# Performance work log

Hardware: AMD Instinct MI355X
Metric: run time of the kernel (lower is better)

Reference implementation:

```python
import jax, jax.numpy as jnp
import numpy as np

EPS = 1e-5  # batch-norm epsilon


def subm_conv(feat, nbrs, W):
    # feat: [N, Cin], nbrs: [N, K] int indices into feat (rulebook), W: [K, Cin, Cout]
    gathered = feat[nbrs]                      # [N, K, Cin]  irregular gather
    return jnp.einsum('nkc,kcd->nd', gathered, W)


def batch_norm(f, gamma, beta):
    # training-mode BN over active sites (scn.BatchNormalization semantics)
    mean = jnp.mean(f, axis=0)
    var = jnp.var(f, axis=0)
    return (f - mean) * jax.lax.rsqrt(var + EPS) * gamma + beta


def setup_inputs() -> dict:
    key = jax.random.key(0)
    k1, k2, k3, k4 = jax.random.split(key, 4)
    N, K, C = 300000, 9, 64
    scale = 1.0 / np.sqrt(K * C)
    return {
        'x': jax.random.normal(k1, (N, C), dtype=jnp.float32),
        'nbrs': jax.random.randint(k2, (N, K), 0, N, dtype=jnp.int32),
        'W1': jax.random.normal(k3, (K, C, C), dtype=jnp.float32) * scale,
        'gamma1': jnp.ones((C,), jnp.float32),
        'beta1': jnp.zeros((C,), jnp.float32),
        'W2': jax.random.normal(k4, (K, C, C), dtype=jnp.float32) * scale,
        'gamma2': jnp.ones((C,), jnp.float32),
        'beta2': jnp.zeros((C,), jnp.float32),
    }


def reference(x, nbrs, W1, gamma1, beta1, W2, gamma2, beta2):
    residual = x
    out = subm_conv(x, nbrs, W1)                       # conv1 (no bias)
    out = jax.nn.relu(batch_norm(out, gamma1, beta1))  # BatchNormReLU
    out = subm_conv(out, nbrs, W2)                     # conv2 (no bias)
    out = batch_norm(out, gamma2, beta2)               # BatchNormalization
    out = jax.nn.relu(out + residual)                  # AddTable + ReLU
    return out
```

## Files before the change

### kernel.cpp

```cpp
#include <hip/hip_runtime.h>

#define NROWS 300000
#define NBLK ((NROWS + 63) / 64)

typedef float f32x4 __attribute__((ext_vector_type(4)));
typedef short s16x8 __attribute__((ext_vector_type(8)));
typedef unsigned short u16x8 __attribute__((ext_vector_type(8)));
typedef unsigned short u16x4 __attribute__((ext_vector_type(4)));

__device__ __forceinline__ float bf2f(unsigned short u) {
    return __uint_as_float(((unsigned)u) << 16);
}
__device__ __forceinline__ unsigned short f2bf(float f) {
    unsigned u = __float_as_uint(f);
    u += 0x7FFFu + ((u >> 16) & 1u);
    return (unsigned short)(u >> 16);
}

__global__ __launch_bounds__(256) void w_prep(const float* __restrict__ W1,
                                              const float* __restrict__ W2,
                                              unsigned short* __restrict__ WT1,
                                              unsigned short* __restrict__ WT2) {
    const int i = blockIdx.x * 256 + threadIdx.x;
    if (i < 9 * 4096) {
        const int k = i >> 12, cc = (i >> 6) & 63, d = i & 63;
        const int o = k * 4096 + d * 64 + cc;
        WT1[o] = f2bf(W1[i]);
        WT2[o] = f2bf(W2[i]);
    }
}

template <int CONV>
__global__ __launch_bounds__(256) void conv_mfma(const float* __restrict__ xf,
                                                 const unsigned short* __restrict__ xb,
                                                 const int* __restrict__ nbrs,
                                                 const unsigned short* __restrict__ WT,
                                                 const float* __restrict__ sb,
                                                 unsigned short* __restrict__ outb) {
    const int tid = threadIdx.x;
    const int l = tid & 63;
    const int w = tid >> 6;
    const int lr = l & 15;
    const int kg = l >> 4;
    const int c00 = kg * 8;

    const int rowA = blockIdx.x * 64 + w * 16 + lr;
    const int rowAc = rowA < NROWS ? rowA : NROWS - 1;

    float sreg[2][8], breg[2][8];
    if (CONV == 2) {
#pragma unroll
        for (int ch = 0; ch < 2; ++ch)
#pragma unroll
            for (int j = 0; j < 8; ++j) {
                sreg[ch][j] = sb[ch * 32 + c00 + j];
                breg[ch][j] = sb[64 + ch * 32 + c00 + j];
            }
    }

    int nb[9];
#pragma unroll
    for (int k = 0; k < 9; ++k) nb[k] = nbrs[rowAc * 9 + k];

    f32x4 acc[4];
#pragma unroll
    for (int d = 0; d < 4; ++d) {
        acc[d][0] = 0.f; acc[d][1] = 0.f; acc[d][2] = 0.f; acc[d][3] = 0.f;
    }

#pragma unroll
    for (int k = 0; k < 9; ++k) {
#pragma unroll
        for (int ch = 0; ch < 2; ++ch) {
            const int c0 = ch * 32 + c00;
            s16x8 a;
            if (CONV == 1) {
                const float* rp = xf + (size_t)nb[k] * 64 + c0;
                const float4 v0 = *(const float4*)rp;
                const float4 v1 = *(const float4*)(rp + 4);
                a[0] = (short)f2bf(v0.x); a[1] = (short)f2bf(v0.y);
                a[2] = (short)f2bf(v0.z); a[3] = (short)f2bf(v0.w);
                a[4] = (short)f2bf(v1.x); a[5] = (short)f2bf(v1.y);
                a[6] = (short)f2bf(v1.z); a[7] = (short)f2bf(v1.w);
            } else {
                const u16x8 raw = *(const u16x8*)(xb + (size_t)nb[k] * 64 + c0);
#pragma unroll
                for (int j = 0; j < 8; ++j) {
                    float f = bf2f(raw[j]);
                    f = fmaxf(f * sreg[ch][j] + breg[ch][j], 0.f);
                    a[j] = (short)f2bf(f);
                }
            }
            const unsigned short* wp = WT + k * 4096 + lr * 64 + c0;
#pragma unroll
            for (int dj = 0; dj < 4; ++dj) {
                const s16x8 b = *(const s16x8*)(wp + dj * 1024);
                acc[dj] = __builtin_amdgcn_mfma_f32_16x16x32_bf16(a, b, acc[dj], 0, 0, 0);
            }
        }
    }

    const int orow0 = blockIdx.x * 64 + w * 16 + kg * 4;
#pragma unroll
    for (int dj = 0; dj < 4; ++dj) {
#pragma unroll
        for (int r = 0; r < 4; ++r) {
            const int orow = orow0 + r;
            if (orow < NROWS) outb[(size_t)orow * 64 + dj * 16 + lr] = f2bf(acc[dj][r]);
        }
    }
}

__global__ __launch_bounds__(256) void bn_stats(const unsigned short* __restrict__ fb,
                                                float* __restrict__ S) {
    const int t = threadIdx.x;
    const int c4 = (t & 15) * 4;
    const int rg = t >> 4;
    float s0 = 0, s1 = 0, s2 = 0, s3 = 0, q0 = 0, q1 = 0, q2 = 0, q3 = 0;
    for (int r = blockIdx.x * 16 + rg; r < NROWS; r += gridDim.x * 16) {
        const u16x4 v = *(const u16x4*)(fb + (size_t)r * 64 + c4);
        const float f0 = bf2f(v[0]), f1 = bf2f(v[1]), f2 = bf2f(v[2]), f3 = bf2f(v[3]);
        s0 += f0; s1 += f1; s2 += f2; s3 += f3;
        q0 += f0 * f0; q1 += f1 * f1; q2 += f2 * f2; q3 += f3 * f3;
    }
    __shared__ float red[16][64];
    red[rg][c4 + 0] = s0; red[rg][c4 + 1] = s1; red[rg][c4 + 2] = s2; red[rg][c4 + 3] = s3;
    __syncthreads();
    if (t < 64) {
        float a = 0;
#pragma unroll
        for (int i = 0; i < 16; ++i) a += red[i][t];
        atomicAdd(&S[t], a);
    }
    __syncthreads();
    red[rg][c4 + 0] = q0; red[rg][c4 + 1] = q1; red[rg][c4 + 2] = q2; red[rg][c4 + 3] = q3;
    __syncthreads();
    if (t < 64) {
        float a = 0;
#pragma unroll
        for (int i = 0; i < 16; ++i) a += red[i][t];
        atomicAdd(&S[64 + t], a);
    }
}

__global__ void bn_finalize(const float* __restrict__ S, const float* __restrict__ gamma,
                            const float* __restrict__ beta, float* __restrict__ sb) {
    const int c = threadIdx.x;
    if (c < 64) {
        const float mean = S[c] * (1.0f / NROWS);
        const float var = S[64 + c] * (1.0f / NROWS) - mean * mean;
        const float sc = gamma[c] * rsqrtf(var + 1e-5f);
        sb[c] = sc;
        sb[64 + c] = beta[c] - mean * sc;
    }
}

__global__ __launch_bounds__(256) void final_out(const unsigned short* __restrict__ o2,
                                                 const float* __restrict__ x,
                                                 const float* __restrict__ sb,
                                                 float* __restrict__ out) {
    const int NQ = NROWS * 16;
    for (int i = blockIdx.x * 256 + threadIdx.x; i < NQ; i += gridDim.x * 256) {
        const int c4 = (i & 15) * 4;
        const u16x4 v = *(const u16x4*)(o2 + (size_t)i * 4);
        const float4 xv = *(const float4*)(x + (size_t)i * 4);
        const float4 s = *(const float4*)(sb + c4);
        const float4 b = *(const float4*)(sb + 64 + c4);
        float4 o;
        o.x = fmaxf(bf2f(v[0]) * s.x + b.x + xv.x, 0.f);
        o.y = fmaxf(bf2f(v[1]) * s.y + b.y + xv.y, 0.f);
        o.z = fmaxf(bf2f(v[2]) * s.z + b.z + xv.z, 0.f);
        o.w = fmaxf(bf2f(v[3]) * s.w + b.w + xv.w, 0.f);
        *(float4*)(out + (size_t)i * 4) = o;
    }
}

extern "C" void kernel_launch(void* const* d_in, const int* in_sizes, int n_in,
                              void* d_out, int out_size, void* d_ws, size_t ws_size,
                              hipStream_t stream) {
    const float* x      = (const float*)d_in[0];
    const int*   nbrs   = (const int*)d_in[1];
    const float* W1     = (const float*)d_in[2];
    const float* gamma1 = (const float*)d_in[3];
    const float* beta1  = (const float*)d_in[4];
    const float* W2     = (const float*)d_in[5];
    const float* gamma2 = (const float*)d_in[6];
    const float* beta2  = (const float*)d_in[7];
    float* out = (float*)d_out;

    char* ws = (char*)d_ws;
    unsigned short* out2b = (unsigned short*)ws;
    unsigned short* WT1   = (unsigned short*)(ws + 38400000);
    unsigned short* WT2   = (unsigned short*)(ws + 38400000 + 73728);
    float* Sa  = (float*)(ws + 38400000 + 147456);
    float* Sb  = Sa + 128;
    float* sb1 = Sa + 256;
    float* sb2 = Sa + 384;
    unsigned short* out1b = (unsigned short*)d_out;

    hipMemsetAsync(Sa, 0, 256 * sizeof(float), stream);
    w_prep<<<144, 256, 0, stream>>>(W1, W2, WT1, WT2);
    conv_mfma<1><<<NBLK, 256, 0, stream>>>(x, nullptr, nbrs, WT1, nullptr, out1b);
    bn_stats<<<512, 256, 0, stream>>>(out1b, Sa);
    bn_finalize<<<1, 64, 0, stream>>>(Sa, gamma1, beta1, sb1);
    conv_mfma<2><<<NBLK, 256, 0, stream>>>(nullptr, out1b, nbrs, WT2, sb1, out2b);
    bn_stats<<<512, 256, 0, stream>>>(out2b, Sb);
    bn_finalize<<<1, 64, 0, stream>>>(Sb, gamma2, beta2, sb2);
    final_out<<<2048, 256, 0, stream>>>(out2b, x, sb2, out);
}
```

Before: 517.2 us.

## Pre-convert gather sources to bf16 and hoist all neighbor loads before MFMA

Adds a pass that converts x to bf16 once, and a separate bn_apply pass that normalizes and ReLUs conv1's output in place. This lets both convolutions gather plain bf16 rows instead of fp32 rows or rows needing per-element BN math. The conv kernel now issues all 18 neighbor-row loads up front so the gathers overlap before the MFMA loop. The cost is two extra streaming passes over the activations and much higher register use from the 18 preloaded vectors, which may reduce occupancy.

```diff
diff --git a/kernel.cpp b/kernel.cpp
--- a/kernel.cpp
+++ b/kernel.cpp
@@ -15,6 +15,19 @@
     unsigned u = __float_as_uint(f);
     u += 0x7FFFu + ((u >> 16) & 1u);
     return (unsigned short)(u >> 16);
+}
+
+__global__ __launch_bounds__(256) void x2bf(const float* __restrict__ x,
+                                            unsigned short* __restrict__ xb) {
+    const int NQ = NROWS * 8;
+    for (int i = blockIdx.x * 256 + threadIdx.x; i < NQ; i += gridDim.x * 256) {
+        const float4 v0 = *(const float4*)(x + (size_t)i * 8);
+        const float4 v1 = *(const float4*)(x + (size_t)i * 8 + 4);
+        u16x8 o;
+        o[0] = f2bf(v0.x); o[1] = f2bf(v0.y); o[2] = f2bf(v0.z); o[3] = f2bf(v0.w);
+        o[4] = f2bf(v1.x); o[5] = f2bf(v1.y); o[6] = f2bf(v1.z); o[7] = f2bf(v1.w);
+        *(u16x8*)(xb + (size_t)i * 8) = o;
+    }
 }
 
 __global__ __launch_bounds__(256) void w_prep(const float* __restrict__ W1,
@@ -30,12 +43,9 @@
     }
 }
 
-template <int CONV>
-__global__ __launch_bounds__(256) void conv_mfma(const float* __restrict__ xf,
-                                                 const unsigned short* __restrict__ xb,
+__global__ __launch_bounds__(256) void conv_mfma(const unsigned short* __restrict__ xb,
                                                  const int* __restrict__ nbrs,
                                                  const unsigned short* __restrict__ WT,
-                                                 const float* __restrict__ sb,
                                                  unsigned short* __restrict__ outb) {
     const int tid = threadIdx.x;
     const int l = tid & 63;
@@ -47,20 +57,17 @@
     const int rowA = blockIdx.x * 64 + w * 16 + lr;
     const int rowAc = rowA < NROWS ? rowA : NROWS - 1;
 
-    float sreg[2][8], breg[2][8];
-    if (CONV == 2) {
-#pragma unroll
-        for (int ch = 0; ch < 2; ++ch)
-#pragma unroll
-            for (int j = 0; j < 8; ++j) {
-                sreg[ch][j] = sb[ch * 32 + c00 + j];
-                breg[ch][j] = sb[64 + ch * 32 + c00 + j];
-            }
-    }
-
     int nb[9];
 #pragma unroll
     for (int k = 0; k < 9; ++k) nb[k] = nbrs[rowAc * 9 + k];
+
+    s16x8 raw0[9], raw1[9];
+#pragma unroll
+    for (int k = 0; k < 9; ++k) {
+        const unsigned short* rp = xb + (size_t)nb[k] * 64 + c00;
+        raw0[k] = *(const s16x8*)rp;
+        raw1[k] = *(const s16x8*)(rp + 32);
+    }
 
     f32x4 acc[4];
 #pragma unroll
@@ -70,33 +77,13 @@
 
 #pragma unroll
     for (int k = 0; k < 9; ++k) {
-#pragma unroll
-        for (int ch = 0; ch < 2; ++ch) {
-            const int c0 = ch * 32 + c00;
-            s16x8 a;
-            if (CONV == 1) {
-                const float* rp = xf + (size_t)nb[k] * 64 + c0;
-                const float4 v0 = *(const float4*)rp;
-                const float4 v1 = *(const float4*)(rp + 4);
-                a[0] = (short)f2bf(v0.x); a[1] = (short)f2bf(v0.y);
-                a[2] = (short)f2bf(v0.z); a[3] = (short)f2bf(v0.w);
-                a[4] = (short)f2bf(v1.x); a[5] = (short)f2bf(v1.y);
-                a[6] = (short)f2bf(v1.z); a[7] = (short)f2bf(v1.w);
-            } else {
-                const u16x8 raw = *(const u16x8*)(xb + (size_t)nb[k] * 64 + c0);
-#pragma unroll
-                for (int j = 0; j < 8; ++j) {
-                    float f = bf2f(raw[j]);
-                    f = fmaxf(f * sreg[ch][j] + breg[ch][j], 0.f);
-                    a[j] = (short)f2bf(f);
-                }
-            }
-            const unsigned short* wp = WT + k * 4096 + lr * 64 + c0;
-#pragma unroll
-            for (int dj = 0; dj < 4; ++dj) {
-                const s16x8 b = *(const s16x8*)(wp + dj * 1024);
-                acc[dj] = __builtin_amdgcn_mfma_f32_16x16x32_bf16(a, b, acc[dj], 0, 0, 0);
-            }
+        const unsigned short* wp = WT + k * 4096 + lr * 64 + c00;
+#pragma unroll
+        for (int dj = 0; dj < 4; ++dj) {
+            const s16x8 b0 = *(const s16x8*)(wp + dj * 1024);
+            const s16x8 b1 = *(const s16x8*)(wp + dj * 1024 + 32);
+            acc[dj] = __builtin_amdgcn_mfma_f32_16x16x32_bf16(raw0[k], b0, acc[dj], 0, 0, 0);
+            acc[dj] = __builtin_amdgcn_mfma_f32_16x16x32_bf16(raw1[k], b1, acc[dj], 0, 0, 0);
         }
     }
 
@@ -152,6 +139,22 @@
         const float sc = gamma[c] * rsqrtf(var + 1e-5f);
         sb[c] = sc;
         sb[64 + c] = beta[c] - mean * sc;
+    }
+}
+
+__global__ __launch_bounds__(256) void bn_apply(unsigned short* __restrict__ fb,
+                                                const float* __restrict__ sb) {
+    const int NQ = NROWS * 8;
+    for (int i = blockIdx.x * 256 + threadIdx.x; i < NQ; i += gridDim.x * 256) {
+        const int c8 = (i & 7) * 8;
+        u16x8 v = *(const u16x8*)(fb + (size_t)i * 8);
+        u16x8 o;
+#pragma unroll
+        for (int j = 0; j < 8; ++j) {
+            const float f = fmaxf(bf2f(v[j]) * sb[c8 + j] + sb[64 + c8 + j], 0.f);
+            o[j] = f2bf(f);
+        }
+        *(u16x8*)(fb + (size_t)i * 8) = o;
     }
 }
 
@@ -197,13 +200,16 @@
     float* sb1 = Sa + 256;
     float* sb2 = Sa + 384;
     unsigned short* out1b = (unsigned short*)d_out;
+    unsigned short* xb    = (unsigned short*)d_out + 19200000;
 
     hipMemsetAsync(Sa, 0, 256 * sizeof(float), stream);
+    x2bf<<<2048, 256, 0, stream>>>(x, xb);
     w_prep<<<144, 256, 0, stream>>>(W1, W2, WT1, WT2);
-    conv_mfma<1><<<NBLK, 256, 0, stream>>>(x, nullptr, nbrs, WT1, nullptr, out1b);
+    conv_mfma<<<NBLK, 256, 0, stream>>>(xb, nbrs, WT1, out1b);
     bn_stats<<<512, 256, 0, stream>>>(out1b, Sa);
     bn_finalize<<<1, 64, 0, stream>>>(Sa, gamma1, beta1, sb1);
-    conv_mfma<2><<<NBLK, 256, 0, stream>>>(nullptr, out1b, nbrs, WT2, sb1, out2b);
+    bn_apply<<<2048, 256, 0, stream>>>(out1b, sb1);
+    conv_mfma<<<NBLK, 256, 0, stream>>>(out1b, nbrs, WT2, out2b);
     bn_stats<<<512, 256, 0, stream>>>(out2b, Sb);
     bn_finalize<<<1, 64, 0, stream>>>(Sb, gamma2, beta2, sb2);
     final_out<<<2048, 256, 0, stream>>>(out2b, x, sb2, out);
```

Result: faster. 504.7 us (-2.4%).
